# Kernel optimization log

Measured on AMD Instinct MI355X. Metric: run time of the kernel, lower is better.

## Reference

```python
import jax, jax.numpy as jnp
import numpy as np

WS = 8          # window_size
NH = 12         # num_heads
DIM = 384
HW = 64         # H = W
EPS = 1e-5


def _relative_position_index(ws):
    coords = np.stack(np.meshgrid(np.arange(ws), np.arange(ws), indexing='ij'), 0).reshape(2, -1)
    rel = coords[:, :, None] - coords[:, None, :]            # (2, ws*ws, ws*ws)
    rel = rel.transpose(1, 2, 0)
    rel[:, :, 0] += ws - 1
    rel[:, :, 1] += ws - 1
    rel[:, :, 0] *= 2 * ws - 1
    return jnp.asarray(rel.sum(-1))                           # (ws*ws, ws*ws) int

REL_IDX = _relative_position_index(WS)


def _layernorm(x, w, b):
    mu = x.mean(-1, keepdims=True)
    var = ((x - mu) ** 2).mean(-1, keepdims=True)
    return (x - mu) * jax.lax.rsqrt(var + EPS) * w + b


def setup_inputs() -> dict:
    key = jax.random.key(0)
    ks = jax.random.split(key, 8)
    d = DIM
    s = lambda fan: 1.0 / np.sqrt(fan)
    return {
        'x': jax.random.normal(ks[0], (8, HW * HW, d), jnp.float32),
        'ln1_w': jnp.ones((d,), jnp.float32),
        'ln1_b': jnp.zeros((d,), jnp.float32),
        'qkv_w': jax.random.normal(ks[1], (d, 3 * d), jnp.float32) * s(d),
        'qkv_b': jax.random.normal(ks[2], (3 * d,), jnp.float32) * 0.02,
        'bias_table': jax.random.normal(ks[3], ((2 * WS - 1) ** 2, NH), jnp.float32) * 0.02,
        'proj_w': jax.random.normal(ks[4], (d, d), jnp.float32) * s(d),
        'proj_b': jnp.zeros((d,), jnp.float32),
        'ln2_w': jnp.ones((d,), jnp.float32),
        'ln2_b': jnp.zeros((d,), jnp.float32),
        'fc1_w': jax.random.normal(ks[5], (d, 4 * d), jnp.float32) * s(d),
        'fc1_b': jnp.zeros((4 * d,), jnp.float32),
        'fc2_w': jax.random.normal(ks[6], (4 * d, d), jnp.float32) * s(4 * d),
        'fc2_b': jnp.zeros((d,), jnp.float32),
    }


def reference(x, ln1_w, ln1_b, qkv_w, qkv_b, bias_table, proj_w, proj_b,
              ln2_w, ln2_b, fc1_w, fc1_b, fc2_w, fc2_b):
    B, N, C = x.shape
    H = W = HW
    Nw = WS * WS
    hd = C // NH

    # window partition: (B, H, W, C) -> (B*nW, ws*ws, C)
    xg = x.reshape(B, H // WS, WS, W // WS, WS, C)
    xw = xg.transpose(0, 1, 3, 2, 4, 5).reshape(-1, Nw, C)

    # --- window attention on LayerNorm'd input ---
    h = _layernorm(xw, ln1_w, ln1_b)
    qkv = (h @ qkv_w + qkv_b).reshape(-1, Nw, 3, NH, hd)
    q, k, v = (qkv[:, :, i].transpose(0, 2, 1, 3) for i in range(3))  # (Bw, NH, Nw, hd)
    attn = jnp.einsum('bhnd,bhmd->bhnm', q, k) * (C ** -0.5)          # NOTE: scale uses full C, as in source
    rel_bias = bias_table[REL_IDX].transpose(2, 0, 1)                  # (NH, Nw, Nw)
    attn = jax.nn.softmax(attn + rel_bias[None], axis=-1)
    out = jnp.einsum('bhnm,bhmd->bhnd', attn, v).transpose(0, 2, 1, 3).reshape(-1, Nw, C)
    xw = xw + (out @ proj_w + proj_b)

    # --- MLP ---
    h2 = _layernorm(xw, ln2_w, ln2_b)
    h2 = jax.nn.gelu(h2 @ fc1_w + fc1_b, approximate=False) @ fc2_w + fc2_b
    xw = xw + h2

    # window reverse: (B*nW, ws*ws, C) -> (B, N, C)
    xr = xw.reshape(B, H // WS, W // WS, WS, WS, C)
    xr = xr.transpose(0, 1, 3, 2, 4, 5).reshape(B, H * W, C)
    return xr
```

## Files before the change

### kernel.cpp

```cpp
#include <hip/hip_runtime.h>
#include <hip/hip_bf16.h>
#include <math.h>

typedef __bf16 bf16x8 __attribute__((ext_vector_type(8)));
typedef float  f32x4  __attribute__((ext_vector_type(4)));

__device__ __forceinline__ unsigned short f2bf(float f) {
    unsigned u = __builtin_bit_cast(unsigned, f);
    unsigned r = u + 0x7FFFu + ((u >> 16) & 1u);
    return (unsigned short)(r >> 16);
}

__device__ __forceinline__ void gll16(const unsigned short* g, unsigned short* l) {
    __builtin_amdgcn_global_load_lds((const __attribute__((address_space(1))) void*)g,
                                     (__attribute__((address_space(3))) void*)l, 16, 0, 0);
}

__global__ void transpose_cast(const float* __restrict__ w, unsigned short* __restrict__ wt,
                               int R, int C) {
    int tid = blockIdx.x * 256 + threadIdx.x;
    if (tid >= R * C) return;
    int c = tid / R, r = tid % R;
    wt[(size_t)c * R + r] = f2bf(w[(size_t)r * C + c]);
}

__global__ void relbias_kernel(const float* __restrict__ btab, float* __restrict__ rb) {
    int tid = blockIdx.x * 256 + threadIdx.x;
    if (tid >= 12 * 64 * 64) return;
    int h = tid >> 12, ij = tid & 4095, i = ij >> 6, j = ij & 63;
    int iy = i >> 3, ix = i & 7, jy = j >> 3, jx = j & 7;
    int idx = (iy - jy + 7) * 15 + (ix - jx + 7);
    rb[tid] = btab[idx * 12 + h];
}

__global__ __launch_bounds__(256) void ln_kernel(const float* __restrict__ x,
                                                 const float* __restrict__ w,
                                                 const float* __restrict__ b,
                                                 unsigned short* __restrict__ out) {
    const int lane = threadIdx.x & 63;
    const size_t tok = (size_t)blockIdx.x * 4 + (threadIdx.x >> 6);
    const float* row = x + tok * 384;
    float v[6];
    float s = 0.f, s2 = 0.f;
#pragma unroll
    for (int j = 0; j < 6; ++j) {
        v[j] = row[lane + j * 64];
        s += v[j]; s2 += v[j] * v[j];
    }
#pragma unroll
    for (int m = 1; m < 64; m <<= 1) { s += __shfl_xor(s, m); s2 += __shfl_xor(s2, m); }
    const float mean = s * (1.f / 384.f);
    const float var  = s2 * (1.f / 384.f) - mean * mean;
    const float inv  = rsqrtf(var + 1e-5f);
#pragma unroll
    for (int j = 0; j < 6; ++j) {
        int c = lane + j * 64;
        out[tok * 384 + c] = f2bf((v[j] - mean) * inv * w[c] + b[c]);
    }
}

template <int EPI, int KT>
__global__ __launch_bounds__(256) void gemm_v5(const unsigned short* __restrict__ A,
                                               const unsigned short* __restrict__ Bt,
                                               const float* __restrict__ bias,
                                               const float* __restrict__ resid,
                                               void* __restrict__ outp, int N) {
    constexpr int K = KT * 32;
    __shared__ char smem[32768];

    const int t = threadIdx.x, lane = t & 63, w = t >> 6;
    const int wm = w >> 1, wn = w & 1, l16 = lane & 15, lk = lane >> 4;

    const int Nt  = N >> 7;
    const int cpx = (int)gridDim.x >> 3;
    const int logical = ((int)blockIdx.x & 7) * cpx + ((int)blockIdx.x >> 3);
    const int n0 = (logical % Nt) * 128;
    const int m0 = (logical / Nt) * 128;

    const int srow = t >> 2;
    const int sch  = t & 3;
    const int ssw  = (srow >> 1) & 3;

    const unsigned short* gsrc[4];
    gsrc[0] = A  + (size_t)(m0 + srow) * K      + (sch ^ ssw) * 8;
    gsrc[1] = A  + (size_t)(m0 + 64 + srow) * K + (sch ^ ssw) * 8;
    gsrc[2] = Bt + (size_t)(n0 + srow) * K      + (sch ^ ssw) * 8;
    gsrc[3] = Bt + (size_t)(n0 + 64 + srow) * K + (sch ^ ssw) * 8;

    unsigned short* ldst0 = (unsigned short*)smem + srow * 32 + sch * 8;

    f32x4 acc[4][4] = {};

    {
        unsigned short* d = ldst0;
        gll16(gsrc[0], d);
        gll16(gsrc[1], d + 2048);
        gll16(gsrc[2], d + 4096);
        gll16(gsrc[3], d + 6144);
    }

#pragma unroll 2
    for (int kt = 0; kt < KT; ++kt) {
        __syncthreads();
        if (kt + 1 < KT) {
            unsigned short* d = ldst0 + ((kt + 1) & 1) * 8192;
            const int go = (kt + 1) * 32;
            gll16(gsrc[0] + go, d);
            gll16(gsrc[1] + go, d + 2048);
            gll16(gsrc[2] + go, d + 4096);
            gll16(gsrc[3] + go, d + 6144);
        }
        const char* sb = smem + (kt & 1) * 16384;
        bf16x8 af[4], bf[4];
#pragma unroll
        for (int mt = 0; mt < 4; ++mt) {
            int row = wm * 64 + mt * 16 + l16;
            af[mt] = *(const bf16x8*)(sb + row * 64 + ((lk ^ ((row >> 1) & 3)) << 4));
        }
#pragma unroll
        for (int nt = 0; nt < 4; ++nt) {
            int row = wn * 64 + nt * 16 + l16;
            bf[nt] = *(const bf16x8*)(sb + 8192 + row * 64 + ((lk ^ ((row >> 1) & 3)) << 4));
        }
#pragma unroll
        for (int mt = 0; mt < 4; ++mt)
#pragma unroll
            for (int nt = 0; nt < 4; ++nt)
                acc[mt][nt] = __builtin_amdgcn_mfma_f32_16x16x32_bf16(
                    af[mt], bf[nt], acc[mt][nt], 0, 0, 0);
    }

    __syncthreads();
    float* eb = (float*)(smem + w * 8192);
    const int colbase = n0 + wn * 64;

#pragma unroll
    for (int p = 0; p < 2; ++p) {
#pragma unroll
        for (int mh = 0; mh < 2; ++mh) {
            int mt = p * 2 + mh;
#pragma unroll
            for (int nt = 0; nt < 4; ++nt) {
                int scol = (nt * 16 + l16) ^ (lk << 4);
#pragma unroll
                for (int r = 0; r < 4; ++r) {
                    int lrow = mh * 16 + lk * 4 + r;
                    eb[lrow * 64 + scol] = acc[mt][nt][r];
                }
            }
        }
#pragma unroll
        for (int s = 0; s < 8; ++s) {
            int lrow = s * 4 + (lane >> 4);
            int col  = (lane & 15) * 4;
            f32x4 v = *(const f32x4*)&eb[lrow * 64 + (col ^ (((lrow >> 2) & 3) << 4))];
            int gcol = colbase + col;
            size_t grow = (size_t)(m0 + wm * 64 + p * 32 + lrow);
            float4 bv = *(const float4*)&bias[gcol];
            v[0] += bv.x; v[1] += bv.y; v[2] += bv.z; v[3] += bv.w;
            if constexpr (EPI == 0) {
                ushort4 o; o.x = f2bf(v[0]); o.y = f2bf(v[1]); o.z = f2bf(v[2]); o.w = f2bf(v[3]);
                *(ushort4*)&((unsigned short*)outp)[grow * N + gcol] = o;
            } else if constexpr (EPI == 1) {
                float4 rv = *(const float4*)&resid[grow * N + gcol];
                float4 o; o.x = rv.x + v[0]; o.y = rv.y + v[1]; o.z = rv.z + v[2]; o.w = rv.w + v[3];
                *(float4*)&((float*)outp)[grow * N + gcol] = o;
            } else if constexpr (EPI == 2) {
                ushort4 o;
                o.x = f2bf(0.5f * v[0] * (1.0f + erff(v[0] * 0.70710678118f)));
                o.y = f2bf(0.5f * v[1] * (1.0f + erff(v[1] * 0.70710678118f)));
                o.z = f2bf(0.5f * v[2] * (1.0f + erff(v[2] * 0.70710678118f)));
                o.w = f2bf(0.5f * v[3] * (1.0f + erff(v[3] * 0.70710678118f)));
                *(ushort4*)&((unsigned short*)outp)[grow * N + gcol] = o;
            } else {
                ushort4 o; o.x = f2bf(v[0]); o.y = f2bf(v[1]); o.z = f2bf(v[2]); o.w = f2bf(v[3]);
                int which = gcol / 384;
                int rem   = gcol - which * 384;
                int head  = rem >> 5, dim = rem & 31;
                size_t addr = ((size_t)(which * 12 + head) * 32768 + grow) * 32 + dim;
                *(ushort4*)&((unsigned short*)outp)[addr] = o;
            }
        }
    }
}

__global__ __launch_bounds__(256) void attn_kernel(const unsigned short* __restrict__ qkv,
                                                   const float* __restrict__ relbias,
                                                   unsigned short* __restrict__ attnout) {
    __shared__ unsigned short sVT[4][2048];
    __shared__ unsigned short sP[4][4096];

    const int t    = threadIdx.x;
    const int lane = t & 63;
    const int w    = t >> 6;
    const int l16  = lane & 15, lk = lane >> 4;

    const int wnd = blockIdx.x / 3;
    const int h   = (blockIdx.x % 3) * 4 + w;

    const int b  = wnd >> 6;
    const int wy = (wnd >> 3) & 7;
    const int wx = wnd & 7;
    const int base_tok = b * 4096 + wy * 512 + wx * 8;

    const unsigned short* Qb = qkv + (size_t)h * (32768 * 32);
    const unsigned short* Kb = qkv + (size_t)(12 + h) * (32768 * 32);
    const unsigned short* Vb = qkv + (size_t)(24 + h) * (32768 * 32);

    bf16x8 qf[4], kf[4];
#pragma unroll
    for (int mt = 0; mt < 4; ++mt) {
        int tok = mt * 16 + l16;
        size_t trow = (size_t)(base_tok + (tok >> 3) * 64 + (tok & 7));
        qf[mt] = *(const bf16x8*)(Qb + trow * 32 + lk * 8);
        kf[mt] = *(const bf16x8*)(Kb + trow * 32 + lk * 8);
    }

    {
        size_t trow = (size_t)(base_tok + (lane >> 3) * 64 + (lane & 7));
        __attribute__((aligned(16))) unsigned short vv[32];
#pragma unroll
        for (int i = 0; i < 4; ++i)
            *(float4*)&vv[i * 8] = *(const float4*)(Vb + trow * 32 + i * 8);
#pragma unroll
        for (int d = 0; d < 32; ++d) {
            int byte = d * 128 + ((lane * 2) ^ ((d & 7) << 4));
            *(unsigned short*)((char*)&sVT[w][0] + byte) = vv[d];
        }
    }

    f32x4 s[4][4] = {};
#pragma unroll
    for (int mt = 0; mt < 4; ++mt)
#pragma unroll
        for (int nt = 0; nt < 4; ++nt)
            s[mt][nt] = __builtin_amdgcn_mfma_f32_16x16x32_bf16(qf[mt], kf[nt], s[mt][nt], 0, 0, 0);

    const float scale = 0.051031036307982884f;
#pragma unroll
    for (int mt = 0; mt < 4; ++mt) {
#pragma unroll
        for (int r = 0; r < 4; ++r) {
            int row = mt * 16 + lk * 4 + r;
            float vals[4];
#pragma unroll
            for (int nt = 0; nt < 4; ++nt)
                vals[nt] = s[mt][nt][r] * scale + relbias[((h * 64) + row) * 64 + nt * 16 + l16];
            float mx = fmaxf(fmaxf(vals[0], vals[1]), fmaxf(vals[2], vals[3]));
            mx = fmaxf(mx, __shfl_xor(mx, 1));
            mx = fmaxf(mx, __shfl_xor(mx, 2));
            mx = fmaxf(mx, __shfl_xor(mx, 4));
            mx = fmaxf(mx, __shfl_xor(mx, 8));
            float sum = 0.f;
#pragma unroll
            for (int nt = 0; nt < 4; ++nt) { vals[nt] = __expf(vals[nt] - mx); sum += vals[nt]; }
            sum += __shfl_xor(sum, 1);
            sum += __shfl_xor(sum, 2);
            sum += __shfl_xor(sum, 4);
            sum += __shfl_xor(sum, 8);
            float inv = 1.0f / sum;
#pragma unroll
            for (int nt = 0; nt < 4; ++nt) {
                int col = nt * 16 + l16;
                int byte = row * 128 + ((col * 2) ^ ((row & 7) << 4));
                *(unsigned short*)((char*)&sP[w][0] + byte) = f2bf(vals[nt] * inv);
            }
        }
    }

    f32x4 o[4][2] = {};
#pragma unroll
    for (int kk = 0; kk < 2; ++kk) {
        bf16x8 pf[4], vf[2];
#pragma unroll
        for (int mt = 0; mt < 4; ++mt) {
            int row = mt * 16 + l16;
            int byte = row * 128 + ((kk * 64 + lk * 16) ^ ((row & 7) << 4));
            pf[mt] = *(const bf16x8*)((const char*)&sP[w][0] + byte);
        }
#pragma unroll
        for (int nt = 0; nt < 2; ++nt) {
            int d = nt * 16 + l16;
            int byte = d * 128 + ((kk * 64 + lk * 16) ^ ((d & 7) << 4));
            vf[nt] = *(const bf16x8*)((const char*)&sVT[w][0] + byte);
        }
#pragma unroll
        for (int mt = 0; mt < 4; ++mt)
#pragma unroll
            for (int nt = 0; nt < 2; ++nt)
                o[mt][nt] = __builtin_amdgcn_mfma_f32_16x16x32_bf16(pf[mt], vf[nt], o[mt][nt], 0, 0, 0);
    }

    float* ob = (float*)&sP[w][0];
#pragma unroll
    for (int mt = 0; mt < 4; ++mt)
#pragma unroll
        for (int nt = 0; nt < 2; ++nt) {
            int dim = (nt * 16 + l16) ^ ((lk & 1) << 4);
#pragma unroll
            for (int r = 0; r < 4; ++r) {
                int tok = mt * 16 + lk * 4 + r;
                ob[tok * 32 + dim] = o[mt][nt][r];
            }
        }
#pragma unroll
    for (int s2 = 0; s2 < 8; ++s2) {
        int tok = s2 * 8 + (lane >> 3);
        int dim = (lane & 7) * 4;
        f32x4 v = *(const f32x4*)&ob[tok * 32 + (dim ^ (((tok >> 2) & 1) << 4))];
        size_t orow = (size_t)(base_tok + (tok >> 3) * 64 + (tok & 7)) * 384 + h * 32 + dim;
        ushort4 ov; ov.x = f2bf(v[0]); ov.y = f2bf(v[1]); ov.z = f2bf(v[2]); ov.w = f2bf(v[3]);
        *(ushort4*)&attnout[orow] = ov;
    }
}

extern "C" void kernel_launch(void* const* d_in, const int* in_sizes, int n_in,
                              void* d_out, int out_size, void* d_ws, size_t ws_size,
                              hipStream_t stream) {
    (void)in_sizes; (void)n_in; (void)out_size; (void)ws_size;
    const float* x      = (const float*)d_in[0];
    const float* ln1_w  = (const float*)d_in[1];
    const float* ln1_b  = (const float*)d_in[2];
    const float* qkv_w  = (const float*)d_in[3];
    const float* qkv_b  = (const float*)d_in[4];
    const float* btab   = (const float*)d_in[5];
    const float* proj_w = (const float*)d_in[6];
    const float* proj_b = (const float*)d_in[7];
    const float* ln2_w  = (const float*)d_in[8];
    const float* ln2_b  = (const float*)d_in[9];
    const float* fc1_w  = (const float*)d_in[10];
    const float* fc1_b  = (const float*)d_in[11];
    const float* fc2_w  = (const float*)d_in[12];
    const float* fc2_b  = (const float*)d_in[13];

    char* p = (char*)d_ws;
    auto alloc = [&](size_t bytes) {
        char* r = p;
        p += (bytes + 255) & ~(size_t)255;
        return r;
    };
    unsigned short* wqkv_t  = (unsigned short*)alloc((size_t)1152 * 384 * 2);
    unsigned short* wproj_t = (unsigned short*)alloc((size_t)384 * 384 * 2);
    unsigned short* wfc1_t  = (unsigned short*)alloc((size_t)1536 * 384 * 2);
    unsigned short* wfc2_t  = (unsigned short*)alloc((size_t)384 * 1536 * 2);
    float*          relbias = (float*)alloc((size_t)12 * 64 * 64 * 4);
    unsigned short* hbuf    = (unsigned short*)alloc((size_t)32768 * 384 * 2);
    unsigned short* bigbuf  = (unsigned short*)alloc((size_t)32768 * 1536 * 2);
    unsigned short* attno   = (unsigned short*)alloc((size_t)32768 * 384 * 2);
    float*          x2      = (float*)alloc((size_t)32768 * 384 * 4);

    const int T = 32768;

    transpose_cast<<<(384 * 1152 + 255) / 256, 256, 0, stream>>>(qkv_w, wqkv_t, 384, 1152);
    transpose_cast<<<(384 * 384 + 255) / 256, 256, 0, stream>>>(proj_w, wproj_t, 384, 384);
    transpose_cast<<<(384 * 1536 + 255) / 256, 256, 0, stream>>>(fc1_w, wfc1_t, 384, 1536);
    transpose_cast<<<(1536 * 384 + 255) / 256, 256, 0, stream>>>(fc2_w, wfc2_t, 1536, 384);
    relbias_kernel<<<(12 * 64 * 64 + 255) / 256, 256, 0, stream>>>(btab, relbias);

    ln_kernel<<<T / 4, 256, 0, stream>>>(x, ln1_w, ln1_b, hbuf);
    gemm_v5<3, 12><<<(1152 / 128) * (T / 128), 256, 0, stream>>>(hbuf, wqkv_t, qkv_b, nullptr,
                                                                 bigbuf, 1152);
    attn_kernel<<<512 * 3, 256, 0, stream>>>(bigbuf, relbias, attno);
    gemm_v5<1, 12><<<(384 / 128) * (T / 128), 256, 0, stream>>>(attno, wproj_t, proj_b, x,
                                                                x2, 384);
    ln_kernel<<<T / 4, 256, 0, stream>>>(x2, ln2_w, ln2_b, hbuf);
    gemm_v5<2, 12><<<(1536 / 128) * (T / 128), 256, 0, stream>>>(hbuf, wfc1_t, fc1_b, nullptr,
                                                                 bigbuf, 1536);
    gemm_v5<1, 48><<<(384 / 128) * (T / 128), 256, 0, stream>>>(bigbuf, wfc2_t, fc2_b, x2,
                                                                (float*)d_out, 384);
}
```

Baseline: 306.3 us.

## Triple-buffer GEMM LDS loads with vmcnt waits and use polynomial erf GELU

The GEMM main loop moves from double to triple buffering in LDS (48KB). It issues loads two k-steps ahead and replaces __syncthreads with an explicit s_waitcnt vmcnt plus s_barrier, so more global-to-LDS latency is hidden. The exact erff in the fc1 GELU epilogue is replaced by the Abramowitz-Stegun polynomial approximation using rcp and exp, which is cheaper but carries about 1e-7 error. The larger LDS footprint may reduce occupancy, and the hand-written waitcnt logic relies on the exact count of outstanding loads.

```diff
diff --git a/kernel.cpp b/kernel.cpp
--- a/kernel.cpp
+++ b/kernel.cpp
@@ -9,6 +9,17 @@
     unsigned u = __builtin_bit_cast(unsigned, f);
     unsigned r = u + 0x7FFFu + ((u >> 16) & 1u);
     return (unsigned short)(r >> 16);
+}
+
+__device__ __forceinline__ float gelu_fast(float v) {
+    float xs = v * 0.70710678118f;
+    float ax = fabsf(xs);
+    float t  = __builtin_amdgcn_rcpf(1.0f + 0.3275911f * ax);
+    float p  = t * (0.254829592f + t * (-0.284496736f + t * (1.421413741f +
+               t * (-1.453152027f + t * 1.061405429f))));
+    float er = 1.0f - p * __expf(-ax * ax);
+    er = copysignf(er, xs);
+    return v * (0.5f + 0.5f * er);
 }
 
 __device__ __forceinline__ void gll16(const unsigned short* g, unsigned short* l) {
@@ -60,13 +71,13 @@
 }
 
 template <int EPI, int KT>
-__global__ __launch_bounds__(256) void gemm_v5(const unsigned short* __restrict__ A,
+__global__ __launch_bounds__(256) void gemm_v6(const unsigned short* __restrict__ A,
                                                const unsigned short* __restrict__ Bt,
                                                const float* __restrict__ bias,
                                                const float* __restrict__ resid,
                                                void* __restrict__ outp, int N) {
     constexpr int K = KT * 32;
-    __shared__ char smem[32768];
+    __shared__ char smem[49152];
 
     const int t = threadIdx.x, lane = t & 63, w = t >> 6;
     const int wm = w >> 1, wn = w & 1, l16 = lane & 15, lk = lane >> 4;
@@ -89,28 +100,28 @@
 
     unsigned short* ldst0 = (unsigned short*)smem + srow * 32 + sch * 8;
 
+    auto stage = [&](int buf, int kk) {
+        unsigned short* d = ldst0 + buf * 8192;
+        const int go = kk * 32;
+        gll16(gsrc[0] + go, d);
+        gll16(gsrc[1] + go, d + 2048);
+        gll16(gsrc[2] + go, d + 4096);
+        gll16(gsrc[3] + go, d + 6144);
+    };
+
     f32x4 acc[4][4] = {};
 
-    {
-        unsigned short* d = ldst0;
-        gll16(gsrc[0], d);
-        gll16(gsrc[1], d + 2048);
-        gll16(gsrc[2], d + 4096);
-        gll16(gsrc[3], d + 6144);
-    }
-
-#pragma unroll 2
+    stage(0, 0);
+    stage(1, 1);
+
+#pragma unroll 3
     for (int kt = 0; kt < KT; ++kt) {
-        __syncthreads();
-        if (kt + 1 < KT) {
-            unsigned short* d = ldst0 + ((kt + 1) & 1) * 8192;
-            const int go = (kt + 1) * 32;
-            gll16(gsrc[0] + go, d);
-            gll16(gsrc[1] + go, d + 2048);
-            gll16(gsrc[2] + go, d + 4096);
-            gll16(gsrc[3] + go, d + 6144);
-        }
-        const char* sb = smem + (kt & 1) * 16384;
+        if (kt + 1 < KT) asm volatile("s_waitcnt vmcnt(4)" ::: "memory");
+        else             asm volatile("s_waitcnt vmcnt(0)" ::: "memory");
+        asm volatile("s_barrier" ::: "memory");
+        if (kt + 2 < KT) stage((kt + 2) % 3, kt + 2);
+
+        const char* sb = smem + (kt % 3) * 16384;
         bf16x8 af[4], bf[4];
 #pragma unroll
         for (int mt = 0; mt < 4; ++mt) {
@@ -167,10 +178,10 @@
                 *(float4*)&((float*)outp)[grow * N + gcol] = o;
             } else if constexpr (EPI == 2) {
                 ushort4 o;
-                o.x = f2bf(0.5f * v[0] * (1.0f + erff(v[0] * 0.70710678118f)));
-                o.y = f2bf(0.5f * v[1] * (1.0f + erff(v[1] * 0.70710678118f)));
-                o.z = f2bf(0.5f * v[2] * (1.0f + erff(v[2] * 0.70710678118f)));
-                o.w = f2bf(0.5f * v[3] * (1.0f + erff(v[3] * 0.70710678118f)));
+                o.x = f2bf(gelu_fast(v[0]));
+                o.y = f2bf(gelu_fast(v[1]));
+                o.z = f2bf(gelu_fast(v[2]));
+                o.w = f2bf(gelu_fast(v[3]));
                 *(ushort4*)&((unsigned short*)outp)[grow * N + gcol] = o;
             } else {
                 ushort4 o; o.x = f2bf(v[0]); o.y = f2bf(v[1]); o.z = f2bf(v[2]); o.w = f2bf(v[3]);
@@ -358,14 +369,14 @@
     relbias_kernel<<<(12 * 64 * 64 + 255) / 256, 256, 0, stream>>>(btab, relbias);
 
     ln_kernel<<<T / 4, 256, 0, stream>>>(x, ln1_w, ln1_b, hbuf);
-    gemm_v5<3, 12><<<(1152 / 128) * (T / 128), 256, 0, stream>>>(hbuf, wqkv_t, qkv_b, nullptr,
+    gemm_v6<3, 12><<<(1152 / 128) * (T / 128), 256, 0, stream>>>(hbuf, wqkv_t, qkv_b, nullptr,
                                                                  bigbuf, 1152);
     attn_kernel<<<512 * 3, 256, 0, stream>>>(bigbuf, relbias, attno);
-    gemm_v5<1, 12><<<(384 / 128) * (T / 128), 256, 0, stream>>>(attno, wproj_t, proj_b, x,
+    gemm_v6<1, 12><<<(384 / 128) * (T / 128), 256, 0, stream>>>(attno, wproj_t, proj_b, x,
                                                                 x2, 384);
     ln_kernel<<<T / 4, 256, 0, stream>>>(x2, ln2_w, ln2_b, hbuf);
-    gemm_v5<2, 12><<<(1536 / 128) * (T / 128), 256, 0, stream>>>(hbuf, wfc1_t, fc1_b, nullptr,
+    gemm_v6<2, 12><<<(1536 / 128) * (T / 128), 256, 0, stream>>>(hbuf, wfc1_t, fc1_b, nullptr,
                                                                  bigbuf, 1536);
-    gemm_v5<1, 48><<<(384 / 128) * (T / 128), 256, 0, stream>>>(bigbuf, wfc2_t, fc2_b, x2,
+    gemm_v6<1, 48><<<(384 / 128) * (T / 128), 256, 0, stream>>>(bigbuf, wfc2_t, fc2_b, x2,
                                                                 (float*)d_out, 384);
 }
```

Result: faster. 290.4 us (-5.2%).
